# Optimization experiments

Hardware: AMD Instinct MI355X
Metric: run time of the kernel (lower is better)

Reference implementation:

```python
import jax, jax.numpy as jnp
import numpy as np

WINDOW = 13

def setup_inputs() -> dict:
    key = jax.random.key(0)
    ks = jax.random.split(key, 5)
    B, C, D, H, W = 8, 64, 13, 64, 64
    c8 = C // 8
    x = jax.random.normal(ks[0], (B, C, D, H, W), dtype=jnp.float32)
    wq = jax.random.normal(ks[1], (c8, C), dtype=jnp.float32) * 0.1
    wk = jax.random.normal(ks[2], (c8, C), dtype=jnp.float32) * 0.1
    wv = jax.random.normal(ks[3], (C, C), dtype=jnp.float32) * 0.1
    bq = jnp.zeros((c8,), jnp.float32)
    bk = jnp.zeros((c8,), jnp.float32)
    bv = jnp.zeros((C,), jnp.float32)
    return {"x": x, "wq": wq, "bq": bq, "wk": wk, "bk": bk, "wv": wv, "bv": bv}

def reference(x, wq, bq, wk, bk, wv, bv):
    B, C, D, H, W = x.shape
    N = D * H * W
    nb = N // WINDOW  # N chosen divisible by WINDOW
    xf = x.reshape(B, C, N)
    # 1x1 Conv3d == per-voxel channel matmul
    q = jnp.einsum('oc,bcn->bon', wq, xf) + bq[None, :, None]
    k = jnp.einsum('oc,bcn->bon', wk, xf) + bk[None, :, None]
    v = jnp.einsum('oc,bcn->bon', wv, xf) + bv[None, :, None]
    # split flattened spatial dim into independent windows of size 13
    qb = q.reshape(B, -1, nb, WINDOW)
    kb = k.reshape(B, -1, nb, WINDOW)
    vb = v.reshape(B, C, nb, WINDOW)
    # scores[b,n,i,j] = sum_c q[b,c,n,i] * k[b,c,n,j]  (no scaling, as in source)
    scores = jnp.einsum('bcni,bcnj->bnij', qb, kb)
    att = jax.nn.softmax(scores, axis=-1)
    # out[b,c,n,i] = sum_j v[b,c,n,j] * att[b,n,i,j]  (v @ att^T per window)
    out = jnp.einsum('bcnj,bnij->bcni', vb, att)
    return out.reshape(B, C, D, H, W)
```

## Files before the change

kernel.cpp:

```cpp
#include <hip/hip_runtime.h>

#define WINDOW 13
#define NTOT   53248
#define WPB    8
#define VT     104
#define VS     112
#define WS     72
#define QKS    112
#define VFS    68

typedef float floatx4 __attribute__((ext_vector_type(4)));
typedef short shortx8 __attribute__((ext_vector_type(8)));

__device__ __forceinline__ unsigned short f2bf(float f) {
    union { float f; unsigned int u; } v; v.f = f;
    unsigned int u = v.u;
    unsigned int r = (u + 0x7fffu + ((u >> 16) & 1u)) >> 16;
    return (unsigned short)r;
}

__global__ __launch_bounds__(256, 4)
void attn_win13_kernel(const float* __restrict__ x,
                       const float* __restrict__ wq, const float* __restrict__ bq,
                       const float* __restrict__ wk, const float* __restrict__ bk,
                       const float* __restrict__ wv, const float* __restrict__ bv,
                       float* __restrict__ out)
{
    __shared__ unsigned short xT[VS * WS];
    __shared__ unsigned short wbf[80 * WS];
    __shared__ float ball[80];
    __shared__ float vf[VS * VFS];
    __shared__ float qk[16 * QKS];
    __shared__ float att[WPB * 169];

    const int tid = threadIdx.x;
    const int b   = blockIdx.y;
    const int v0  = blockIdx.x * VT;
    const size_t total = (size_t)512 * NTOT;

    for (int f = tid; f < 1280; f += 256) {
        const int r = f >> 4, c = (f & 15) * 4;
        const float* src = (r < 8)  ? (wq + r * 64 + c)
                         : (r < 16) ? (wk + (r - 8) * 64 + c)
                                    : (wv + (r - 16) * 64 + c);
        const float4 w4 = *(const float4*)src;
        *(unsigned int*)(&wbf[r * WS + c])     = (unsigned int)f2bf(w4.x) | ((unsigned int)f2bf(w4.y) << 16);
        *(unsigned int*)(&wbf[r * WS + c + 2]) = (unsigned int)f2bf(w4.z) | ((unsigned int)f2bf(w4.w) << 16);
    }
    if (tid < 80)
        ball[tid] = (tid < 8) ? bq[tid] : (tid < 16) ? bk[tid - 8] : bv[tid - 16];

    for (int f = tid; f < 896; f += 256) {
        const int cp = f / 28, vq = f % 28;
        const int c = cp * 2, vx = vq * 4;
        size_t i0 = (size_t)(b * 64 + c) * NTOT + v0 + vx;
        size_t i1 = i0 + NTOT;
        if (i0 > total - 4) i0 = total - 4;
        if (i1 > total - 4) i1 = total - 4;
        const float4 x0 = *(const float4*)(x + i0);
        const float4 x1 = *(const float4*)(x + i1);
        *(unsigned int*)(&xT[(vx + 0) * WS + c]) = (unsigned int)f2bf(x0.x) | ((unsigned int)f2bf(x1.x) << 16);
        *(unsigned int*)(&xT[(vx + 1) * WS + c]) = (unsigned int)f2bf(x0.y) | ((unsigned int)f2bf(x1.y) << 16);
        *(unsigned int*)(&xT[(vx + 2) * WS + c]) = (unsigned int)f2bf(x0.z) | ((unsigned int)f2bf(x1.z) << 16);
        *(unsigned int*)(&xT[(vx + 3) * WS + c]) = (unsigned int)f2bf(x0.w) | ((unsigned int)f2bf(x1.w) << 16);
    }
    __syncthreads();

    {
        const int wid  = tid >> 6;
        const int lane = tid & 63;
        const int col  = lane & 15;
        const int g    = lane >> 4;
        for (int t = wid; t < 35; t += 4) {
            const int mt = t / 7, nt = t % 7;
            const shortx8 a0 = *(const shortx8*)(&wbf[(mt * 16 + col) * WS + g * 8]);
            const shortx8 b0 = *(const shortx8*)(&xT [(nt * 16 + col) * WS + g * 8]);
            const shortx8 a1 = *(const shortx8*)(&wbf[(mt * 16 + col) * WS + 32 + g * 8]);
            const shortx8 b1 = *(const shortx8*)(&xT [(nt * 16 + col) * WS + 32 + g * 8]);
            floatx4 acc = {0.f, 0.f, 0.f, 0.f};
            acc = __builtin_amdgcn_mfma_f32_16x16x32_bf16(a0, b0, acc, 0, 0, 0);
            acc = __builtin_amdgcn_mfma_f32_16x16x32_bf16(a1, b1, acc, 0, 0, 0);
            const int row0 = mt * 16 + g * 4;
            const int vox  = nt * 16 + col;
            if (mt == 0) {
                qk[(row0 + 0) * QKS + vox] = acc[0] + ball[row0 + 0];
                qk[(row0 + 1) * QKS + vox] = acc[1] + ball[row0 + 1];
                qk[(row0 + 2) * QKS + vox] = acc[2] + ball[row0 + 2];
                qk[(row0 + 3) * QKS + vox] = acc[3] + ball[row0 + 3];
            } else {
                const int c0 = row0 - 16;
                float4 st = make_float4(acc[0] + ball[row0 + 0], acc[1] + ball[row0 + 1],
                                        acc[2] + ball[row0 + 2], acc[3] + ball[row0 + 3]);
                *(float4*)(&vf[vox * VFS + c0]) = st;
            }
        }
    }
    __syncthreads();

    for (int f = tid; f < WPB * 169; f += 256) {
        const int w = f / 169, rem = f % 169;
        const int i = rem / 13, j = rem % 13;
        const float* qp = &qk[w * 13 + i];
        const float* kp = &qk[w * 13 + j];
        float s = 0.f;
#pragma unroll
        for (int o = 0; o < 8; ++o)
            s += qp[o * QKS] * kp[(8 + o) * QKS];
        att[f] = s;
    }
    __syncthreads();

    if (tid < WPB * WINDOW) {
        float* row = att + tid * 13;
        float m = row[0];
#pragma unroll
        for (int j = 1; j < 13; ++j) m = fmaxf(m, row[j]);
        float s0 = __expf(row[0] - m), s1 = __expf(row[1] - m), s2 = __expf(row[2] - m);
        float s3 = __expf(row[3] - m), s4 = __expf(row[4] - m), s5 = __expf(row[5] - m);
        float s6 = __expf(row[6] - m), s7 = __expf(row[7] - m), s8 = __expf(row[8] - m);
        float s9 = __expf(row[9] - m), sa = __expf(row[10] - m), sb = __expf(row[11] - m);
        float sc = __expf(row[12] - m);
        const float inv = 1.f / (s0+s1+s2+s3+s4+s5+s6+s7+s8+s9+sa+sb+sc);
        row[0]=s0*inv; row[1]=s1*inv; row[2]=s2*inv; row[3]=s3*inv; row[4]=s4*inv;
        row[5]=s5*inv; row[6]=s6*inv; row[7]=s7*inv; row[8]=s8*inv; row[9]=s9*inv;
        row[10]=sa*inv; row[11]=sb*inv; row[12]=sc*inv;
    }
    __syncthreads();

    for (int f = tid; f < 16 * VT; f += 256) {
        const int cg = f / VT, vx = f % VT;
        const int w = vx / 13, i = vx % 13;
        const float* arow  = att + w * 169 + i * 13;
        const float* vbase = &vf[(w * 13) * VFS + cg * 4];
        float4 o4 = make_float4(0.f, 0.f, 0.f, 0.f);
#pragma unroll
        for (int j = 0; j < 13; ++j) {
            const float a = arow[j];
            const float4 vv = *(const float4*)(vbase + j * VFS);
            o4.x += a * vv.x; o4.y += a * vv.y; o4.z += a * vv.z; o4.w += a * vv.w;
        }
        float* op = out + (size_t)(b * 64 + cg * 4) * NTOT + v0 + vx;
        op[0]                 = o4.x;
        op[(size_t)NTOT]      = o4.y;
        op[(size_t)2 * NTOT]  = o4.z;
        op[(size_t)3 * NTOT]  = o4.w;
    }
}

extern "C" void kernel_launch(void* const* d_in, const int* in_sizes, int n_in,
                              void* d_out, int out_size, void* d_ws, size_t ws_size,
                              hipStream_t stream) {
    const float* x  = (const float*)d_in[0];
    const float* wq = (const float*)d_in[1];
    const float* bq = (const float*)d_in[2];
    const float* wk = (const float*)d_in[3];
    const float* bk = (const float*)d_in[4];
    const float* wv = (const float*)d_in[5];
    const float* bv = (const float*)d_in[6];
    float* out = (float*)d_out;

    dim3 grid(NTOT / VT, 8);
    dim3 block(256);
    attn_win13_kernel<<<grid, block, 0, stream>>>(x, wq, bq, wk, bk, wv, bv, out);
}
```

Baseline: 258.3 us.

## Double block size and split x/weight staging across thread halves

Raises the block to 512 threads and gives the x transpose-and-convert load to the first 224 threads and the weight conversion to threads 256 and up, so the two staging jobs run concurrently. Each x thread now loads 8 channels and writes one 16-byte packed bf16 vector instead of 4-byte stores. The later loops stride by 512 and the MFMA tile loop uses 8 waves. Larger blocks can lower occupancy given the shared memory per block, and all threads still wait at the same barriers, with the 35 MFMA tiles spread unevenly over 8 waves.

```diff
diff --git a/kernel.cpp b/kernel.cpp
--- a/kernel.cpp
+++ b/kernel.cpp
@@ -19,17 +19,21 @@
     return (unsigned short)r;
 }
 
-__global__ __launch_bounds__(256, 4)
+__device__ __forceinline__ unsigned int pk2(float a, float b) {
+    return (unsigned int)f2bf(a) | ((unsigned int)f2bf(b) << 16);
+}
+
+__global__ __launch_bounds__(512, 4)
 void attn_win13_kernel(const float* __restrict__ x,
                        const float* __restrict__ wq, const float* __restrict__ bq,
                        const float* __restrict__ wk, const float* __restrict__ bk,
                        const float* __restrict__ wv, const float* __restrict__ bv,
                        float* __restrict__ out)
 {
-    __shared__ unsigned short xT[VS * WS];
-    __shared__ unsigned short wbf[80 * WS];
+    __shared__ __align__(16) unsigned short xT[VS * WS];
+    __shared__ __align__(16) unsigned short wbf[80 * WS];
     __shared__ float ball[80];
-    __shared__ float vf[VS * VFS];
+    __shared__ __align__(16) float vf[VS * VFS];
     __shared__ float qk[16 * QKS];
     __shared__ float att[WPB * 169];
 
@@ -38,31 +42,48 @@
     const int v0  = blockIdx.x * VT;
     const size_t total = (size_t)512 * NTOT;
 
-    for (int f = tid; f < 1280; f += 256) {
-        const int r = f >> 4, c = (f & 15) * 4;
-        const float* src = (r < 8)  ? (wq + r * 64 + c)
-                         : (r < 16) ? (wk + (r - 8) * 64 + c)
-                                    : (wv + (r - 16) * 64 + c);
-        const float4 w4 = *(const float4*)src;
-        *(unsigned int*)(&wbf[r * WS + c])     = (unsigned int)f2bf(w4.x) | ((unsigned int)f2bf(w4.y) << 16);
-        *(unsigned int*)(&wbf[r * WS + c + 2]) = (unsigned int)f2bf(w4.z) | ((unsigned int)f2bf(w4.w) << 16);
+    if (tid < 224) {
+        const int vq = tid >> 3, cg8 = tid & 7;
+        const int c0 = cg8 * 8, vx = vq * 4;
+        float xv[4][8];
+#pragma unroll
+        for (int i = 0; i < 8; ++i) {
+            size_t idx = (size_t)(b * 64 + c0 + i) * NTOT + v0 + vx;
+            if (idx > total - 4) idx = total - 4;
+            const float4 t = *(const float4*)(x + idx);
+            xv[0][i] = t.x; xv[1][i] = t.y; xv[2][i] = t.z; xv[3][i] = t.w;
+        }
+#pragma unroll
+        for (int r = 0; r < 4; ++r) {
+            uint4 pk;
+            pk.x = pk2(xv[r][0], xv[r][1]);
+            pk.y = pk2(xv[r][2], xv[r][3]);
+            pk.z = pk2(xv[r][4], xv[r][5]);
+            pk.w = pk2(xv[r][6], xv[r][7]);
+            *(uint4*)(&xT[(vx + r) * WS + c0]) = pk;
+        }
+    } else if (tid >= 256) {
+        const int wf0 = tid - 256;
+#pragma unroll
+        for (int it = 0; it < 3; ++it) {
+            const int wf = wf0 + (it << 8);
+            if (wf < 640) {
+                const int r = wf >> 3, cw = (wf & 7) * 8;
+                const float* src = (r < 8)  ? (wq + r * 64 + cw)
+                                 : (r < 16) ? (wk + (r - 8) * 64 + cw)
+                                            : (wv + (r - 16) * 64 + cw);
+                const float4 w0 = *(const float4*)src;
+                const float4 w1 = *(const float4*)(src + 4);
+                uint4 pk;
+                pk.x = pk2(w0.x, w0.y); pk.y = pk2(w0.z, w0.w);
+                pk.z = pk2(w1.x, w1.y); pk.w = pk2(w1.z, w1.w);
+                *(uint4*)(&wbf[r * WS + cw]) = pk;
+            }
+        }
     }
-    if (tid < 80)
-        ball[tid] = (tid < 8) ? bq[tid] : (tid < 16) ? bk[tid - 8] : bv[tid - 16];
-
-    for (int f = tid; f < 896; f += 256) {
-        const int cp = f / 28, vq = f % 28;
-        const int c = cp * 2, vx = vq * 4;
-        size_t i0 = (size_t)(b * 64 + c) * NTOT + v0 + vx;
-        size_t i1 = i0 + NTOT;
-        if (i0 > total - 4) i0 = total - 4;
-        if (i1 > total - 4) i1 = total - 4;
-        const float4 x0 = *(const float4*)(x + i0);
-        const float4 x1 = *(const float4*)(x + i1);
-        *(unsigned int*)(&xT[(vx + 0) * WS + c]) = (unsigned int)f2bf(x0.x) | ((unsigned int)f2bf(x1.x) << 16);
-        *(unsigned int*)(&xT[(vx + 1) * WS + c]) = (unsigned int)f2bf(x0.y) | ((unsigned int)f2bf(x1.y) << 16);
-        *(unsigned int*)(&xT[(vx + 2) * WS + c]) = (unsigned int)f2bf(x0.z) | ((unsigned int)f2bf(x1.z) << 16);
-        *(unsigned int*)(&xT[(vx + 3) * WS + c]) = (unsigned int)f2bf(x0.w) | ((unsigned int)f2bf(x1.w) << 16);
+    if (tid >= 432) {
+        const int t2 = tid - 432;
+        ball[t2] = (t2 < 8) ? bq[t2] : (t2 < 16) ? bk[t2 - 8] : bv[t2 - 16];
     }
     __syncthreads();
 
@@ -71,7 +92,7 @@
         const int lane = tid & 63;
         const int col  = lane & 15;
         const int g    = lane >> 4;
-        for (int t = wid; t < 35; t += 4) {
+        for (int t = wid; t < 35; t += 8) {
             const int mt = t / 7, nt = t % 7;
             const shortx8 a0 = *(const shortx8*)(&wbf[(mt * 16 + col) * WS + g * 8]);
             const shortx8 b0 = *(const shortx8*)(&xT [(nt * 16 + col) * WS + g * 8]);
@@ -97,7 +118,7 @@
     }
     __syncthreads();
 
-    for (int f = tid; f < WPB * 169; f += 256) {
+    for (int f = tid; f < WPB * 169; f += 512) {
         const int w = f / 169, rem = f % 169;
         const int i = rem / 13, j = rem % 13;
         const float* qp = &qk[w * 13 + i];
@@ -127,7 +148,7 @@
     }
     __syncthreads();
 
-    for (int f = tid; f < 16 * VT; f += 256) {
+    for (int f = tid; f < 16 * VT; f += 512) {
         const int cg = f / VT, vx = f % VT;
         const int w = vx / 13, i = vx % 13;
         const float* arow  = att + w * 169 + i * 13;
@@ -160,6 +181,6 @@
     float* out = (float*)d_out;
 
     dim3 grid(NTOT / VT, 8);
-    dim3 block(256);
+    dim3 block(512);
     attn_win13_kernel<<<grid, block, 0, stream>>>(x, wq, bq, wk, bk, wv, bv, out);
 }
```

Result: faster. 235.7 us (-8.8%).
